# Performance work log

Measured on AMD Instinct MI355X. Metric: run time of the kernel, lower is better.

Reference implementation:

```python
import jax, jax.numpy as jnp
import numpy as np

N = 100000   # nodes
E = 1600000  # edges (avg degree 16), self-loops added in reference
H = 64       # hidden


def setup_inputs() -> dict:
    key = jax.random.key(0)
    k1, k2, k3, k4, k5 = jax.random.split(key, 5)
    x = jax.random.normal(k1, (N, H), dtype=jnp.float32)
    src = jax.random.randint(k2, (E,), 0, N, dtype=jnp.int32)
    off = jax.random.randint(k3, (E,), 1, N, dtype=jnp.int32)
    dst = (src + off) % N  # guaranteed no self-loops -> matches add_remaining_self_loops
    edge_index = jnp.stack([src, dst])  # row0 = j (source), row1 = i (target)
    # a_i, a_j: Linear(hidden, 1, bias=False) -> weight vectors of shape [H]
    w_i = jax.random.normal(k4, (H,), dtype=jnp.float32) / np.sqrt(H)
    w_j = jax.random.normal(k5, (H,), dtype=jnp.float32) / np.sqrt(H)
    return {"x": x, "edge_index": edge_index, "w_i": w_i, "w_j": w_j}


def reference(x, edge_index, w_i, w_j):
    n = x.shape[0]
    # add_remaining_self_loops: append (v, v) for every node (inputs have none)
    loops = jnp.arange(n, dtype=edge_index.dtype)
    src = jnp.concatenate([edge_index[0], loops])  # j
    dst = jnp.concatenate([edge_index[1], loops])  # i
    # per-node attention scalars, then per-edge gather
    s_i = x @ w_i  # [N]
    s_j = x @ w_j  # [N]
    e = jax.nn.leaky_relu(s_i[dst] + s_j[src], 0.01)  # [E+N]
    # segment softmax over destination node i (every segment non-empty via self-loop)
    e_max = jax.ops.segment_max(e, dst, num_segments=n)
    e_exp = jnp.exp(e - e_max[dst])
    denom = jax.ops.segment_sum(e_exp, dst, num_segments=n)
    alpha = e_exp / denom[dst]  # [E+N]
    # spmm: out[i] = sum_j alpha_ij * x[j], then ReLU
    out = jax.ops.segment_sum(alpha[:, None] * x[src], dst, num_segments=n)
    return jax.nn.relu(out)
```

## Files before the change

kernel.cpp:

```cpp
#include <hip/hip_runtime.h>

#define H 64
#define H4 16
#define H8 8
#define NBUCK 391
#define CAP 4608
#define BIN_BLOCKS 196
#define NODE_PER_BLK 16

typedef _Float16 half8 __attribute__((ext_vector_type(8)));


__global__ __launch_bounds__(1024) void gat_nodebin_kernel(
        const float* __restrict__ x,
        const float* __restrict__ w_i, const float* __restrict__ w_j,
        float* __restrict__ s_i, float* __restrict__ s_j,
        _Float16* __restrict__ xh,
        const int4* __restrict__ src4, const int4* __restrict__ dst4,
        int* __restrict__ cursor, int* __restrict__ buckets,
        int e4, int n) {
    __shared__ int hist[NBUCK];
    __shared__ int boff[NBUCK];
    __shared__ int boff0[NBUCK];
    __shared__ int gbase[NBUCK];
    __shared__ int wtot[16];
    __shared__ int stage[8192];

    int tid = threadIdx.x;
    int lane = tid & 63, wv = tid >> 6;

    if (blockIdx.x >= BIN_BLOCKS) {
        int node = (blockIdx.x - BIN_BLOCKS) * NODE_PER_BLK + wv;
        if (node >= n) return;
        float v = x[(long long)node * H + lane];
        xh[(long long)node * H + lane] = (_Float16)v;
        float a = v * w_i[lane];
        float b = v * w_j[lane];
        #pragma unroll
        for (int off = 32; off > 0; off >>= 1) {
            a += __shfl_down(a, off, 64);
            b += __shfl_down(b, off, 64);
        }
        if (lane == 0) { s_i[node] = a; s_j[node] = b; }
        return;
    }

    if (tid < NBUCK) hist[tid] = 0;
    __syncthreads();

    int4 s[2], d[2];
    bool val[2];
    #pragma unroll
    for (int r = 0; r < 2; ++r) {
        int i4 = blockIdx.x * 2048 + r * 1024 + tid;
        val[r] = (i4 < e4);
        if (val[r]) { s[r] = src4[i4]; d[r] = dst4[i4]; }
        else        { s[r] = make_int4(0,0,0,0); d[r] = make_int4(0,0,0,0); }
    }
    #pragma unroll
    for (int r = 0; r < 2; ++r) if (val[r]) {
        atomicAdd(&hist[d[r].x >> 8], 1);
        atomicAdd(&hist[d[r].y >> 8], 1);
        atomicAdd(&hist[d[r].z >> 8], 1);
        atomicAdd(&hist[d[r].w >> 8], 1);
    }
    __syncthreads();

    if (tid < NBUCK) gbase[tid] = atomicAdd(&cursor[tid], hist[tid]);

    int v = (tid < NBUCK) ? hist[tid] : 0;
    int incl = v;
    #pragma unroll
    for (int off = 1; off < 64; off <<= 1) {
        int t = __shfl_up(incl, off, 64);
        if (lane >= off) incl += t;
    }
    if (lane == 63) wtot[wv] = incl;
    __syncthreads();
    if (tid < NBUCK) {
        int wpref = 0;
        #pragma unroll
        for (int j = 0; j < 16; ++j) wpref += (j < wv) ? wtot[j] : 0;
        int excl = wpref + incl - v;
        boff[tid]  = excl;
        boff0[tid] = excl;
    }
    __syncthreads();

    #pragma unroll
    for (int r = 0; r < 2; ++r) if (val[r]) {
        int ss[4] = {s[r].x, s[r].y, s[r].z, s[r].w};
        int dd[4] = {d[r].x, d[r].y, d[r].z, d[r].w};
        #pragma unroll
        for (int c = 0; c < 4; ++c) {
            int b = dd[c] >> 8;
            int pos = atomicAdd(&boff[b], 1);
            stage[pos] = ((dd[c] & 255) << 17) | ss[c];
        }
    }
    __syncthreads();

    for (int b = wv; b < NBUCK; b += 16) {
        int sbase = boff0[b];
        int L = boff[b] - sbase;
        int gb = gbase[b];
        int* dstp = buckets + (long long)b * CAP + gb;
        for (int i = lane; i < L; i += 64)
            dstp[i] = stage[sbase + i];
    }
}

__global__ __launch_bounds__(512, 4) void gat_sortagg_kernel(
        const float4* __restrict__ x4,
        const half8* __restrict__ xh8,
        const float* __restrict__ s_i,
        const float* __restrict__ s_j,
        const int* __restrict__ cursor,
        const int* __restrict__ buckets,
        float4* __restrict__ out4, int n) {
    __shared__ int   hist[256];
    __shared__ int   offs[256];
    __shared__ int   start0[256];
    __shared__ float sii[256];
    __shared__ int   wtot[8];
    __shared__ int2  ew[CAP];

    int b = blockIdx.x;
    int tid = threadIdx.x;
    int lane = tid & 63, wv = tid >> 6;
    int cnt_b = cursor[b];
    if (cnt_b > CAP) cnt_b = CAP;
    const int* bk = buckets + (long long)b * CAP;

    if (tid < 256) {
        hist[tid] = 0;
        int node = (b << 8) + tid;
        sii[tid] = (node < n) ? s_i[node] : 0.f;
    }
    __syncthreads();

    for (int i = tid; i < cnt_b; i += 512)
        atomicAdd(&hist[(bk[i] >> 17) & 255], 1);
    __syncthreads();

    int v = (tid < 256) ? hist[tid] : 0;
    int incl = v;
    #pragma unroll
    for (int off = 1; off < 64; off <<= 1) {
        int t = __shfl_up(incl, off, 64);
        if (lane >= off) incl += t;
    }
    if (tid < 256 && lane == 63) wtot[wv] = incl;
    __syncthreads();
    if (tid < 256) {
        int wpref = 0;
        #pragma unroll
        for (int j = 0; j < 4; ++j) wpref += (j < wv) ? wtot[j] : 0;
        int excl = wpref + incl - v;
        offs[tid]   = excl;
        start0[tid] = excl;
    }
    __syncthreads();

    for (int i = tid; i < cnt_b; i += 512) {
        int w = bk[i];
        int loc = (w >> 17) & 255;
        int src = w & 0x1FFFF;
        float e = sii[loc] + s_j[src];
        e = (e >= 0.f) ? e : 0.01f * e;
        float we = __expf(e);
        int pos = atomicAdd(&offs[loc], 1);
        ew[pos] = make_int2(src, __float_as_int(we));
    }
    __syncthreads();

    int sub = lane >> 4;
    int g2  = (lane >> 3) & 1;
    int q   = lane & 7;

    for (int rr = 0; rr < 8; ++rr) {
        int loc  = rr * 32 + wv * 4 + sub;
        int node = (b << 8) + loc;
        bool vnode = (node < n);
        int ls   = start0[loc];
        int cntn = vnode ? hist[loc] : 0;

        float acc[8];
        #pragma unroll
        for (int i = 0; i < 8; ++i) acc[i] = 0.f;
        float den = 0.f;

        for (int base = 0; base < cntn; base += 16) {
            int rem = cntn - base;
            int lsb = ls + base + g2;
            if (rem >= 16) {
                int sb[8]; float wb[8]; half8 hv[8];
                #pragma unroll
                for (int j = 0; j < 8; ++j) {
                    int2 e = ew[lsb + 2 * j];
                    sb[j] = e.x; wb[j] = __int_as_float(e.y);
                }
                #pragma unroll
                for (int j = 0; j < 8; ++j)
                    hv[j] = xh8[(long long)sb[j] * H8 + q];
                #pragma unroll
                for (int j = 0; j < 8; ++j) {
                    #pragma unroll
                    for (int i = 0; i < 8; ++i)
                        acc[i] = fmaf(wb[j], (float)hv[j][i], acc[i]);
                    den += wb[j];
                }
            } else {
                int sb[8]; float wb[8]; half8 hv[8];
                #pragma unroll
                for (int j = 0; j < 8; ++j) {
                    int slot = g2 + 2 * j;
                    sb[j] = -1; wb[j] = 0.f;
                    if (slot < rem) {
                        int2 e = ew[lsb + 2 * j];
                        sb[j] = e.x; wb[j] = __int_as_float(e.y);
                    }
                }
                #pragma unroll
                for (int j = 0; j < 8; ++j)
                    if (sb[j] >= 0)
                        hv[j] = xh8[(long long)sb[j] * H8 + q];
                #pragma unroll
                for (int j = 0; j < 8; ++j) {
                    if (sb[j] >= 0) {
                        #pragma unroll
                        for (int i = 0; i < 8; ++i)
                            acc[i] = fmaf(wb[j], (float)hv[j][i], acc[i]);
                        den += wb[j];
                    }
                }
            }
        }

        #pragma unroll
        for (int i = 0; i < 8; ++i) acc[i] += __shfl_xor(acc[i], 8, 64);
        den += __shfl_xor(den, 8, 64);

        if (vnode && g2 == 0) {
            float sjn = s_j[node];
            float e0 = sii[loc] + sjn; e0 = (e0 >= 0.f) ? e0 : 0.01f * e0;
            float w0 = __expf(e0);
            float4 xa = x4[(long long)node * H4 + 2 * q];
            float4 xb = x4[(long long)node * H4 + 2 * q + 1];
            float dinv = 1.f / (den + w0);
            float4 oa, ob;
            oa.x = (acc[0] + w0 * xa.x) * dinv;
            oa.y = (acc[1] + w0 * xa.y) * dinv;
            oa.z = (acc[2] + w0 * xa.z) * dinv;
            oa.w = (acc[3] + w0 * xa.w) * dinv;
            ob.x = (acc[4] + w0 * xb.x) * dinv;
            ob.y = (acc[5] + w0 * xb.y) * dinv;
            ob.z = (acc[6] + w0 * xb.z) * dinv;
            ob.w = (acc[7] + w0 * xb.w) * dinv;
            oa.x = (oa.x > 0.f) ? oa.x : 0.f;
            oa.y = (oa.y > 0.f) ? oa.y : 0.f;
            oa.z = (oa.z > 0.f) ? oa.z : 0.f;
            oa.w = (oa.w > 0.f) ? oa.w : 0.f;
            ob.x = (ob.x > 0.f) ? ob.x : 0.f;
            ob.y = (ob.y > 0.f) ? ob.y : 0.f;
            ob.z = (ob.z > 0.f) ? ob.z : 0.f;
            ob.w = (ob.w > 0.f) ? ob.w : 0.f;
            out4[(long long)node * H4 + 2 * q]     = oa;
            out4[(long long)node * H4 + 2 * q + 1] = ob;
        }
    }
}

extern "C" void kernel_launch(void* const* d_in, const int* in_sizes, int n_in,
                              void* d_out, int out_size, void* d_ws, size_t ws_size,
                              hipStream_t stream) {
    const float* x    = (const float*)d_in[0];
    const int*   edge = (const int*)  d_in[1];
    const float* w_i  = (const float*)d_in[2];
    const float* w_j  = (const float*)d_in[3];

    int n     = in_sizes[0] / H;
    int e_cnt = in_sizes[1] / 2;
    const int* src = edge;
    const int* dst = edge + e_cnt;

    float* out = (float*)d_out;

    char* ws = (char*)d_ws;
    float*    s_i       = (float*)ws;     ws += (size_t)n * 4;
    float*    s_j       = (float*)ws;     ws += (size_t)n * 4;
    int*      cursor    = (int*)ws;       ws += 512 * 4;
    int*      buckets   = (int*)ws;       ws += (size_t)NBUCK * CAP * 4;
    _Float16* xh        = (_Float16*)ws;

    int e4 = e_cnt / 4;
    int node_blocks = (n + NODE_PER_BLK - 1) / NODE_PER_BLK;
    int fused_blocks = BIN_BLOCKS + node_blocks;

    hipMemsetAsync(cursor, 0, 512 * 4, stream);

    gat_nodebin_kernel<<<fused_blocks, 1024, 0, stream>>>(
        x, w_i, w_j, s_i, s_j, xh,
        (const int4*)src, (const int4*)dst, cursor, buckets, e4, n);

    gat_sortagg_kernel<<<NBUCK, 512, 0, stream>>>(
        (const float4*)x, (const half8*)xh, s_i, s_j, cursor, buckets,
        (float4*)out, n);
}
```

Measured before the change: 151.5 us.

## Rebucket destinations into 512 narrower buckets and vectorize node projection

Destination buckets shrink from 256 to 196 nodes, giving 512 buckets, so the aggregation kernel launches more blocks with a smaller shared edge buffer (CAP 3712), which may raise occupancy and balance work across CUs. The binning kernel now handles half as many edges per block across 391 blocks and uses division by the bucket width instead of a shift. The node projection path uses float4 loads, processes four nodes per wave and writes half4 vectors. Risks include the cost of integer division and bucket overflow if a bucket exceeds the smaller capacity.

```diff
diff --git a/kernel.cpp b/kernel.cpp
--- a/kernel.cpp
+++ b/kernel.cpp
@@ -3,17 +3,19 @@
 #define H 64
 #define H4 16
 #define H8 8
-#define NBUCK 391
-#define CAP 4608
-#define BIN_BLOCKS 196
-#define NODE_PER_BLK 16
+#define BWID 196
+#define NBUCK 512
+#define CAP 3712
+#define BIN_BLOCKS 391
+#define NODE_PER_BLK 64
 
 typedef _Float16 half8 __attribute__((ext_vector_type(8)));
+typedef _Float16 half4v __attribute__((ext_vector_type(4)));
 
 
 __global__ __launch_bounds__(1024) void gat_nodebin_kernel(
-        const float* __restrict__ x,
-        const float* __restrict__ w_i, const float* __restrict__ w_j,
+        const float4* __restrict__ x4,
+        const float4* __restrict__ wi4, const float4* __restrict__ wj4,
         float* __restrict__ s_i, float* __restrict__ s_j,
         _Float16* __restrict__ xh,
         const int4* __restrict__ src4, const int4* __restrict__ dst4,
@@ -23,46 +25,46 @@
     __shared__ int boff[NBUCK];
     __shared__ int boff0[NBUCK];
     __shared__ int gbase[NBUCK];
-    __shared__ int wtot[16];
-    __shared__ int stage[8192];
+    __shared__ int wtot[8];
+    __shared__ int stage[4096];
 
     int tid = threadIdx.x;
     int lane = tid & 63, wv = tid >> 6;
 
     if (blockIdx.x >= BIN_BLOCKS) {
-        int node = (blockIdx.x - BIN_BLOCKS) * NODE_PER_BLK + wv;
+        int l16 = lane & 15, nsub = lane >> 4;
+        int node = (blockIdx.x - BIN_BLOCKS) * NODE_PER_BLK + wv * 4 + nsub;
         if (node >= n) return;
-        float v = x[(long long)node * H + lane];
-        xh[(long long)node * H + lane] = (_Float16)v;
-        float a = v * w_i[lane];
-        float b = v * w_j[lane];
-        #pragma unroll
-        for (int off = 32; off > 0; off >>= 1) {
-            a += __shfl_down(a, off, 64);
-            b += __shfl_down(b, off, 64);
+        float4 v = x4[(long long)node * H4 + l16];
+        float4 wi = wi4[l16], wj = wj4[l16];
+        float a = v.x * wi.x + v.y * wi.y + v.z * wi.z + v.w * wi.w;
+        float b = v.x * wj.x + v.y * wj.y + v.z * wj.z + v.w * wj.w;
+        half4v hv;
+        hv[0] = (_Float16)v.x; hv[1] = (_Float16)v.y;
+        hv[2] = (_Float16)v.z; hv[3] = (_Float16)v.w;
+        *(half4v*)(xh + (long long)node * H + l16 * 4) = hv;
+        #pragma unroll
+        for (int m = 1; m <= 8; m <<= 1) {
+            a += __shfl_xor(a, m, 64);
+            b += __shfl_xor(b, m, 64);
         }
-        if (lane == 0) { s_i[node] = a; s_j[node] = b; }
+        if (l16 == 0) { s_i[node] = a; s_j[node] = b; }
         return;
     }
 
     if (tid < NBUCK) hist[tid] = 0;
     __syncthreads();
 
-    int4 s[2], d[2];
-    bool val[2];
-    #pragma unroll
-    for (int r = 0; r < 2; ++r) {
-        int i4 = blockIdx.x * 2048 + r * 1024 + tid;
-        val[r] = (i4 < e4);
-        if (val[r]) { s[r] = src4[i4]; d[r] = dst4[i4]; }
-        else        { s[r] = make_int4(0,0,0,0); d[r] = make_int4(0,0,0,0); }
-    }
-    #pragma unroll
-    for (int r = 0; r < 2; ++r) if (val[r]) {
-        atomicAdd(&hist[d[r].x >> 8], 1);
-        atomicAdd(&hist[d[r].y >> 8], 1);
-        atomicAdd(&hist[d[r].z >> 8], 1);
-        atomicAdd(&hist[d[r].w >> 8], 1);
+    int i4 = blockIdx.x * 1024 + tid;
+    bool val = (i4 < e4);
+    int4 s = val ? src4[i4] : make_int4(0, 0, 0, 0);
+    int4 d = val ? dst4[i4] : make_int4(0, 0, 0, 0);
+    int b0 = d.x / BWID, b1 = d.y / BWID, b2 = d.z / BWID, b3 = d.w / BWID;
+    if (val) {
+        atomicAdd(&hist[b0], 1);
+        atomicAdd(&hist[b1], 1);
+        atomicAdd(&hist[b2], 1);
+        atomicAdd(&hist[b3], 1);
     }
     __syncthreads();
 
@@ -75,28 +77,24 @@
         int t = __shfl_up(incl, off, 64);
         if (lane >= off) incl += t;
     }
-    if (lane == 63) wtot[wv] = incl;
+    if (tid < NBUCK && lane == 63) wtot[wv] = incl;
     __syncthreads();
     if (tid < NBUCK) {
         int wpref = 0;
         #pragma unroll
-        for (int j = 0; j < 16; ++j) wpref += (j < wv) ? wtot[j] : 0;
+        for (int j = 0; j < 8; ++j) wpref += (j < wv) ? wtot[j] : 0;
         int excl = wpref + incl - v;
         boff[tid]  = excl;
         boff0[tid] = excl;
     }
     __syncthreads();
 
-    #pragma unroll
-    for (int r = 0; r < 2; ++r) if (val[r]) {
-        int ss[4] = {s[r].x, s[r].y, s[r].z, s[r].w};
-        int dd[4] = {d[r].x, d[r].y, d[r].z, d[r].w};
-        #pragma unroll
-        for (int c = 0; c < 4; ++c) {
-            int b = dd[c] >> 8;
-            int pos = atomicAdd(&boff[b], 1);
-            stage[pos] = ((dd[c] & 255) << 17) | ss[c];
-        }
+    if (val) {
+        int pos;
+        pos = atomicAdd(&boff[b0], 1); stage[pos] = ((d.x - b0 * BWID) << 17) | s.x;
+        pos = atomicAdd(&boff[b1], 1); stage[pos] = ((d.y - b1 * BWID) << 17) | s.y;
+        pos = atomicAdd(&boff[b2], 1); stage[pos] = ((d.z - b2 * BWID) << 17) | s.z;
+        pos = atomicAdd(&boff[b3], 1); stage[pos] = ((d.w - b3 * BWID) << 17) | s.w;
     }
     __syncthreads();
 
@@ -122,7 +120,7 @@
     __shared__ int   offs[256];
     __shared__ int   start0[256];
     __shared__ float sii[256];
-    __shared__ int   wtot[8];
+    __shared__ int   wtot[4];
     __shared__ int2  ew[CAP];
 
     int b = blockIdx.x;
@@ -134,8 +132,8 @@
 
     if (tid < 256) {
         hist[tid] = 0;
-        int node = (b << 8) + tid;
-        sii[tid] = (node < n) ? s_i[node] : 0.f;
+        int node = b * BWID + tid;
+        sii[tid] = (tid < BWID && node < n) ? s_i[node] : 0.f;
     }
     __syncthreads();
 
@@ -178,12 +176,13 @@
     int g2  = (lane >> 3) & 1;
     int q   = lane & 7;
 
-    for (int rr = 0; rr < 8; ++rr) {
+    for (int rr = 0; rr < 7; ++rr) {
         int loc  = rr * 32 + wv * 4 + sub;
-        int node = (b << 8) + loc;
-        bool vnode = (node < n);
-        int ls   = start0[loc];
-        int cntn = vnode ? hist[loc] : 0;
+        int node = b * BWID + loc;
+        bool vnode = (loc < BWID) && (node < n);
+        int lsafe = vnode ? loc : 0;
+        int ls   = start0[lsafe];
+        int cntn = vnode ? hist[lsafe] : 0;
 
         float acc[8];
         #pragma unroll
@@ -300,7 +299,8 @@
     hipMemsetAsync(cursor, 0, 512 * 4, stream);
 
     gat_nodebin_kernel<<<fused_blocks, 1024, 0, stream>>>(
-        x, w_i, w_j, s_i, s_j, xh,
+        (const float4*)x, (const float4*)w_i, (const float4*)w_j,
+        s_i, s_j, xh,
         (const int4*)src, (const int4*)dst, cursor, buckets, e4, n);
 
     gat_sortagg_kernel<<<NBUCK, 512, 0, stream>>>(
```

Measured after the change: 144.8 us. -4.4%, faster.
